# Kernel tuning notes

Hardware: AMD Instinct MI355X
Metric: run time of the kernel (lower is better)

## Reference

```python
import jax, jax.numpy as jnp
import numpy as np

N_G = 1024
H, W = 192, 256
FX, FY, CX, CY = 220.0, 220.0, 128.0, 96.0
NEAR, FAR = 0.01, 10.0
MARGIN = 0.1
ALPHA_THR = 1e-5
C0 = 0.28209479177387814
C1 = 0.4886025119029199
C2 = (1.0925484305920792, -1.0925484305920792, 0.31539156525252005, -1.0925484305920792, 0.5462742152960396)
C3 = (-0.5900435899266435, 2.890611442640554, -0.4570457994644658, 0.3731763325901154, -0.4570457994644658, 1.445305721320277, -0.5900435899266435)


def setup_inputs() -> dict:
    key = jax.random.key(0)
    k = jax.random.split(key, 6)
    xy = jax.random.uniform(k[0], (N_G, 2), minval=-1.5, maxval=1.5)
    z = jax.random.uniform(k[1], (N_G, 1), minval=0.5, maxval=6.0)
    positions = jnp.concatenate([xy, z], axis=1)
    rotations = jax.random.normal(k[2], (N_G, 4))
    scales = jnp.log(jax.random.uniform(k[3], (N_G, 3), minval=0.02, maxval=0.1))  # log-scale, as in module
    opacity = jax.random.uniform(k[4], (N_G, 1), minval=0.1, maxval=0.9)
    sh_coeffs = 0.3 * jax.random.normal(k[5], (N_G, 16, 3))
    T_WC = jnp.eye(4, dtype=jnp.float32)
    return {"positions": positions, "rotations": rotations, "scales": scales,
            "opacity": opacity, "sh_coeffs": sh_coeffs, "T_WC": T_WC}


def _quat_to_rot(q):
    q = q / (jnp.linalg.norm(q, axis=1, keepdims=True) + 1e-12)
    w, x, y, z = q[:, 0], q[:, 1], q[:, 2], q[:, 3]
    R = jnp.stack([
        1 - 2 * (y * y + z * z), 2 * (x * y - w * z), 2 * (x * z + w * y),
        2 * (x * y + w * z), 1 - 2 * (x * x + z * z), 2 * (y * z - w * x),
        2 * (x * z - w * y), 2 * (y * z + w * x), 1 - 2 * (x * x + y * y)], axis=1)
    return R.reshape(-1, 3, 3)


def _eval_sh(sh, d):
    # sh: [N,16,3] degree-3 SH, d: [N,3] unit view dirs (standard 3DGS real SH)
    x, y, z = d[:, 0:1], d[:, 1:2], d[:, 2:3]
    c = C0 * sh[:, 0] - C1 * y * sh[:, 1] + C1 * z * sh[:, 2] - C1 * x * sh[:, 3]
    xx, yy, zz = x * x, y * y, z * z
    xy, yz, xz = x * y, y * z, x * z
    c = c + C2[0] * xy * sh[:, 4] + C2[1] * yz * sh[:, 5] + C2[2] * (2 * zz - xx - yy) * sh[:, 6] \
          + C2[3] * xz * sh[:, 7] + C2[4] * (xx - yy) * sh[:, 8]
    c = c + C3[0] * y * (3 * xx - yy) * sh[:, 9] + C3[1] * xy * z * sh[:, 10] \
          + C3[2] * y * (4 * zz - xx - yy) * sh[:, 11] + C3[3] * z * (2 * zz - 3 * xx - 3 * yy) * sh[:, 12] \
          + C3[4] * x * (4 * zz - xx - yy) * sh[:, 13] + C3[5] * z * (xx - yy) * sh[:, 14] \
          + C3[6] * x * (xx - 3 * yy) * sh[:, 15]
    return jnp.clip(c + 0.5, 0.0, 1.0)


def _forward(positions, rotations, scales, opacity, sh_coeffs, T_WC):
    n = positions.shape[0]
    pts_h = jnp.concatenate([positions, jnp.ones((n, 1), positions.dtype)], axis=1)
    pc = (pts_h @ T_WC.T)[:, :3]  # world -> camera
    xs_c, ys_c, z = pc[:, 0], pc[:, 1], pc[:, 2]
    az = jnp.abs(z)
    x_fac = max(CX / FX, (W - CX) / FX)
    y_fac = max(CY / FY, (H - CY) / FY)
    valid = (az > NEAR) & (az < FAR) \
        & (jnp.abs(xs_c) < az * x_fac * (1 + MARGIN)) \
        & (jnp.abs(ys_c) < az * y_fac * (1 + MARGIN))
    zs = jnp.where(jnp.abs(z) < 1e-8, 1e-8, z)
    u = FX * xs_c / zs + CX
    v = FY * ys_c / zs + CY
    # 3D covariance Sigma = (R S)(R S)^T, then 2D via perspective Jacobian J Sigma J^T
    R = _quat_to_rot(rotations)
    S = jnp.exp(scales)  # scales stored in log space
    M = R * S[:, None, :]
    cov3d = jnp.einsum('nij,nkj->nik', M, M)
    zero = jnp.zeros_like(zs)
    J = jnp.stack([
        jnp.stack([FX / zs, zero, -FX * xs_c / (zs * zs)], axis=1),
        jnp.stack([zero, FY / zs, -FY * ys_c / (zs * zs)], axis=1)], axis=1)
    cov2d = jnp.einsum('nij,njk,nlk->nil', J, cov3d, J)
    a = cov2d[:, 0, 0] + 0.3  # low-pass dilation as in 3DGS
    b = cov2d[:, 0, 1]
    c = cov2d[:, 1, 1] + 0.3
    det = jnp.maximum(a * c - b * b, 1e-12)
    A, B, Cc = c / det, -b / det, a / det  # conic (inverse covariance)
    # frustum culling as mask: culled gaussians contribute zero opacity
    op = opacity[:, 0] * valid.astype(positions.dtype)
    dirs = pc / (jnp.linalg.norm(pc, axis=1, keepdims=True) + 1e-12)
    colors = _eval_sh(sh_coeffs, dirs)  # [N,3]
    # depth sort DESCENDING (as in module) -> back-to-front painter compositing
    order = jnp.argsort(-z)
    u, v, A, B, Cc, op, zd, colors = (t[order] for t in (u, v, A, B, Cc, op, z, colors))
    # dense per-pixel evaluation  [P, N]
    px = jnp.arange(W, dtype=positions.dtype) + 0.5
    py = jnp.arange(H, dtype=positions.dtype) + 0.5
    gx, gy = jnp.meshgrid(px, py)  # [H, W]
    gx, gy = gx.reshape(-1, 1), gy.reshape(-1, 1)
    dx = gx - u[None, :]
    dy = gy - v[None, :]
    power = -0.5 * (A[None, :] * dx * dx + Cc[None, :] * dy * dy) - B[None, :] * dx * dy
    alpha = jnp.minimum(0.99, op[None, :] * jnp.exp(jnp.minimum(power, 0.0)))
    alpha = jnp.where(alpha < ALPHA_THR, 0.0, alpha)
    # back-to-front: C = sum_i c_i a_i prod_{j>i} (1-a_j)  (exclusive suffix product)
    one_m = 1.0 - alpha
    cp = jnp.cumprod(one_m[:, ::-1], axis=1)
    T = jnp.concatenate([jnp.ones((alpha.shape[0], 1), alpha.dtype), cp[:, :-1]], axis=1)[:, ::-1]
    w = alpha * T
    rgb = (w @ colors).reshape(H, W, 3)
    depth = (w @ zd).reshape(H, W, 1)
    return rgb, depth


def reference(positions, rotations, scales, opacity, sh_coeffs, T_WC):
    return _forward(positions, rotations, scales, opacity, sh_coeffs, T_WC)
```

## Files before the change

### kernel.cpp

```cpp
#include <hip/hip_runtime.h>
#include <hip/hip_bf16.h>

#define NG 1024
#define IMW 256
#define IMH 192
#define NPIX (IMW*IMH)
#define FXc 220.0f
#define FYc 220.0f
#define CXc 128.0f
#define CYc 96.0f
#define NEARc 0.01f
#define FARc 10.0f
#define ALPHA_THRc 1e-5f

#define SH_C0 0.28209479177387814f
#define SH_C1 0.4886025119029199f
#define SH_C2_0 1.0925484305920792f
#define SH_C2_1 (-1.0925484305920792f)
#define SH_C2_2 0.31539156525252005f
#define SH_C2_3 (-1.0925484305920792f)
#define SH_C2_4 0.5462742152960396f
#define SH_C3_0 (-0.5900435899266435f)
#define SH_C3_1 2.890611442640554f
#define SH_C3_2 (-0.4570457994644658f)
#define SH_C3_3 0.3731763325901154f
#define SH_C3_4 (-0.4570457994644658f)
#define SH_C3_5 1.445305721320277f
#define SH_C3_6 (-0.5900435899266435f)


__global__ __launch_bounds__(64)
void gs_prep(const float* __restrict__ pos, const float* __restrict__ rot,
             const float* __restrict__ scl, const float* __restrict__ opac,
             const float* __restrict__ sh,  const float* __restrict__ Twc,
             float4* __restrict__ g0, float4* __restrict__ g1,
             float4* __restrict__ g2) {
    int i = blockIdx.x * 64 + threadIdx.x;
    if (i >= NG) return;

    float p0 = pos[i*3+0], p1 = pos[i*3+1], p2 = pos[i*3+2];
    float xc = Twc[0]*p0 + Twc[1]*p1 + Twc[2]*p2  + Twc[3];
    float yc = Twc[4]*p0 + Twc[5]*p1 + Twc[6]*p2  + Twc[7];
    float zc = Twc[8]*p0 + Twc[9]*p1 + Twc[10]*p2 + Twc[11];

    float az = fabsf(zc);
    const float xfac = fmaxf(CXc/FXc, (IMW - CXc)/FXc) * 1.1f;
    const float yfac = fmaxf(CYc/FYc, (IMH - CYc)/FYc) * 1.1f;
    bool valid = (az > NEARc) && (az < FARc) &&
                 (fabsf(xc) < az * xfac) && (fabsf(yc) < az * yfac);

    float zs = (az < 1e-8f) ? 1e-8f : zc;
    float iz = 1.0f / zs;
    float u = FXc * xc * iz + CXc;
    float v = FYc * yc * iz + CYc;

    float qw = rot[i*4+0], qx = rot[i*4+1], qy = rot[i*4+2], qz = rot[i*4+3];
    float qn = sqrtf(qw*qw + qx*qx + qy*qy + qz*qz) + 1e-12f;
    float inq = 1.0f / qn;
    qw *= inq; qx *= inq; qy *= inq; qz *= inq;
    float R00 = 1.0f - 2.0f*(qy*qy + qz*qz);
    float R01 = 2.0f*(qx*qy - qw*qz);
    float R02 = 2.0f*(qx*qz + qw*qy);
    float R10 = 2.0f*(qx*qy + qw*qz);
    float R11 = 1.0f - 2.0f*(qx*qx + qz*qz);
    float R12 = 2.0f*(qy*qz - qw*qx);
    float R20 = 2.0f*(qx*qz - qw*qy);
    float R21 = 2.0f*(qy*qz + qw*qx);
    float R22 = 1.0f - 2.0f*(qx*qx + qy*qy);

    float s0 = expf(scl[i*3+0]);
    float s1 = expf(scl[i*3+1]);
    float s2 = expf(scl[i*3+2]);
    float M00 = R00*s0, M01 = R01*s1, M02 = R02*s2;
    float M10 = R10*s0, M11 = R11*s1, M12 = R12*s2;
    float M20 = R20*s0, M21 = R21*s1, M22 = R22*s2;

    float S00 = M00*M00 + M01*M01 + M02*M02;
    float S01 = M00*M10 + M01*M11 + M02*M12;
    float S02 = M00*M20 + M01*M21 + M02*M22;
    float S11 = M10*M10 + M11*M11 + M12*M12;
    float S12 = M10*M20 + M11*M21 + M12*M22;
    float S22 = M20*M20 + M21*M21 + M22*M22;

    float j00 = FXc * iz,  j02 = -FXc * xc * iz * iz;
    float j11 = FYc * iz,  j12 = -FYc * yc * iz * iz;
    float c00 = j00*j00*S00 + 2.0f*j00*j02*S02 + j02*j02*S22 + 0.3f;
    float c01 = j00*j11*S01 + j00*j12*S02 + j02*j11*S12 + j02*j12*S22;
    float c11 = j11*j11*S11 + 2.0f*j11*j12*S12 + j12*j12*S22 + 0.3f;
    float det = fmaxf(c00*c11 - c01*c01, 1e-12f);
    float idet = 1.0f / det;
    float Ai = c11 * idet;
    float Bi = -c01 * idet;
    float Ci = c00 * idet;

    float op = valid ? opac[i] : 0.0f;

    float Q = fmaxf(2.0f * logf(fmaxf(op, 1e-20f) * 1e5f), 0.0f);
    float rx = valid ? (sqrtf(Q * c00) + 1e-3f) : -1e9f;
    float ry = valid ? (sqrtf(Q * c11) + 1e-3f) : -1e9f;

    float pn = sqrtf(xc*xc + yc*yc + zc*zc) + 1e-12f;
    float ipn = 1.0f / pn;
    float dx = xc*ipn, dy = yc*ipn, dz = zc*ipn;
    float xx = dx*dx, yy = dy*dy, zz = dz*dz;
    float xy = dx*dy, yz = dy*dz, xz = dx*dz;

    const float* s = sh + i*48;
    float col[3];
#pragma unroll
    for (int ch = 0; ch < 3; ++ch) {
        float c = SH_C0*s[0+ch] - SH_C1*dy*s[3+ch] + SH_C1*dz*s[6+ch] - SH_C1*dx*s[9+ch];
        c += SH_C2_0*xy*s[12+ch] + SH_C2_1*yz*s[15+ch] + SH_C2_2*(2.0f*zz-xx-yy)*s[18+ch]
           + SH_C2_3*xz*s[21+ch] + SH_C2_4*(xx-yy)*s[24+ch];
        c += SH_C3_0*dy*(3.0f*xx-yy)*s[27+ch] + SH_C3_1*xy*dz*s[30+ch]
           + SH_C3_2*dy*(4.0f*zz-xx-yy)*s[33+ch] + SH_C3_3*dz*(2.0f*zz-3.0f*xx-3.0f*yy)*s[36+ch]
           + SH_C3_4*dx*(4.0f*zz-xx-yy)*s[39+ch] + SH_C3_5*dz*(xx-yy)*s[42+ch]
           + SH_C3_6*dx*(xx-3.0f*yy)*s[45+ch];
        col[ch] = fminf(fmaxf(c + 0.5f, 0.0f), 1.0f);
    }

    g0[i] = make_float4(u, v, Ai, Bi);
    g1[i] = make_float4(Ci, op, col[0], col[1]);
    g2[i] = make_float4(col[2], zc, rx, ry);
}

__global__ __launch_bounds__(256)
void gs_tile(const float4* __restrict__ g0, const float4* __restrict__ g1,
             const float4* __restrict__ g2, float* __restrict__ out) {
    __shared__ float4 sv0[NG], sv1[NG], sv2[NG];
    __shared__ unsigned long long key[NG];
    __shared__ unsigned short ord[NG];
    __shared__ int scnt;

    int t = threadIdx.y * 16 + threadIdx.x;
    if (t == 0) scnt = 0;
    __syncthreads();

    float tx0 = (float)(blockIdx.x * 16) + 0.5f;
    float tx1 = tx0 + 15.0f;
    float ty0 = (float)(blockIdx.y * 16) + 0.5f;
    float ty1 = ty0 + 15.0f;

#pragma unroll
    for (int p = 0; p < 4; ++p) {
        int i = p * 256 + t;
        float4 a0 = g0[i];
        float4 a2 = g2[i];
        bool pass = (a0.x + a2.z >= tx0) && (a0.x - a2.z <= tx1) &&
                    (a0.y + a2.w >= ty0) && (a0.y - a2.w <= ty1);
        if (pass) {
            int pos = atomicAdd(&scnt, 1);
            sv0[pos] = a0;
            sv1[pos] = g1[i];
            sv2[pos] = a2;
            unsigned int zb = __float_as_uint(a2.y);
            zb = (zb & 0x80000000u) ? ~zb : (zb | 0x80000000u);
            key[pos] = ((unsigned long long)zb << 32) | (unsigned int)(NG - 1 - i);
        }
    }
    __syncthreads();
    int M = scnt;

    for (int s = t; s < M; s += 256) {
        unsigned long long ks = key[s];
        int rank = 0;
        for (int j = 0; j < M; ++j)
            rank += (key[j] < ks) ? 1 : 0;
        ord[rank] = (unsigned short)s;
    }
    __syncthreads();

    float px = tx0 + (float)threadIdx.x;
    float py = ty0 + (float)threadIdx.y;
    float T = 1.0f;
    float cr = 0.0f, cg = 0.0f, cb = 0.0f, cd = 0.0f;

#pragma unroll 2
    for (int j = 0; j < M; ++j) {
        int slot = ord[j];
        float4 a0 = sv0[slot];
        float4 a1 = sv1[slot];
        float4 a2 = sv2[slot];
        float dx = px - a0.x;
        float dy = py - a0.y;
        float pw = -0.5f * (a0.z * dx * dx + a1.x * dy * dy) - a0.w * dx * dy;
        pw = fminf(pw, 0.0f);
        float alpha = fminf(0.99f, a1.y * __expf(pw));
        float aeff = (alpha >= ALPHA_THRc) ? alpha : 0.0f;
        float w = aeff * T;
        cr += w * a1.z;
        cg += w * a1.w;
        cb += w * a2.x;
        cd += w * a2.y;
        T *= 1.0f - aeff;
        if (__all(T < 1e-4f)) break;
    }

    int x = blockIdx.x * 16 + threadIdx.x;
    int y = blockIdx.y * 16 + threadIdx.y;
    int idx = y * IMW + x;
    out[idx*3 + 0] = cr;
    out[idx*3 + 1] = cg;
    out[idx*3 + 2] = cb;
    out[NPIX*3 + idx] = cd;
}

extern "C" void kernel_launch(void* const* d_in, const int* in_sizes, int n_in,
                              void* d_out, int out_size, void* d_ws, size_t ws_size,
                              hipStream_t stream) {
    const float* pos  = (const float*)d_in[0];
    const float* rot  = (const float*)d_in[1];
    const float* scl  = (const float*)d_in[2];
    const float* opac = (const float*)d_in[3];
    const float* sh   = (const float*)d_in[4];
    const float* Twc  = (const float*)d_in[5];
    float* out = (float*)d_out;

    char* ws = (char*)d_ws;
    float4* g0 = (float4*)ws;
    float4* g1 = (float4*)(ws + 16384);
    float4* g2 = (float4*)(ws + 32768);

    gs_prep<<<dim3(NG/64), dim3(64), 0, stream>>>(pos, rot, scl, opac, sh, Twc,
                                                  g0, g1, g2);
    gs_tile<<<dim3(IMW/16, IMH/16), dim3(16, 16), 0, stream>>>(g0, g1, g2, out);
}
```

Baseline: 27.99 us.

## Use 8x8 single-wavefront tiles and pack colors/depth as fp16

Shrinks tiles from 16x16 pixels with 256 threads to 8x8 pixels with one 64-thread wavefront, giving 768 blocks instead of 192 so more of the GPU is busy. Smaller tiles also cull more Gaussians per tile and let early termination via __all apply per wavefront. Color and depth are packed as half2 into the second float4, removing the third shared array and one LDS load per Gaussian. The fp16 depth also feeds the sort key, which loses precision, can change back-to-front ordering, and lowers the accuracy of the depth output.

```diff
diff --git a/kernel.cpp b/kernel.cpp
--- a/kernel.cpp
+++ b/kernel.cpp
@@ -1,5 +1,6 @@
 #include <hip/hip_runtime.h>
 #include <hip/hip_bf16.h>
+#include <hip/hip_fp16.h>
 
 #define NG 1024
 #define IMW 256
@@ -34,7 +35,7 @@
              const float* __restrict__ scl, const float* __restrict__ opac,
              const float* __restrict__ sh,  const float* __restrict__ Twc,
              float4* __restrict__ g0, float4* __restrict__ g1,
-             float4* __restrict__ g2) {
+             float2* __restrict__ g2) {
     int i = blockIdx.x * 64 + threadIdx.x;
     if (i >= NG) return;
 
@@ -119,41 +120,45 @@
         col[ch] = fminf(fmaxf(c + 0.5f, 0.0f), 1.0f);
     }
 
+    __half2 rg = __floats2half2_rn(col[0], col[1]);
+    __half2 bz = __floats2half2_rn(col[2], zc);
+
     g0[i] = make_float4(u, v, Ai, Bi);
-    g1[i] = make_float4(Ci, op, col[0], col[1]);
-    g2[i] = make_float4(col[2], zc, rx, ry);
+    g1[i] = make_float4(Ci, op, __uint_as_float(*(unsigned int*)&rg),
+                                __uint_as_float(*(unsigned int*)&bz));
+    g2[i] = make_float2(rx, ry);
 }
 
-__global__ __launch_bounds__(256)
+__global__ __launch_bounds__(64)
 void gs_tile(const float4* __restrict__ g0, const float4* __restrict__ g1,
-             const float4* __restrict__ g2, float* __restrict__ out) {
-    __shared__ float4 sv0[NG], sv1[NG], sv2[NG];
+             const float2* __restrict__ g2, float* __restrict__ out) {
+    __shared__ float4 sv0[NG], sv1[NG];
     __shared__ unsigned long long key[NG];
     __shared__ unsigned short ord[NG];
     __shared__ int scnt;
 
-    int t = threadIdx.y * 16 + threadIdx.x;
+    int t = threadIdx.x;
     if (t == 0) scnt = 0;
     __syncthreads();
 
-    float tx0 = (float)(blockIdx.x * 16) + 0.5f;
-    float tx1 = tx0 + 15.0f;
-    float ty0 = (float)(blockIdx.y * 16) + 0.5f;
-    float ty1 = ty0 + 15.0f;
-
-#pragma unroll
-    for (int p = 0; p < 4; ++p) {
-        int i = p * 256 + t;
+    float tx0 = (float)(blockIdx.x * 8) + 0.5f;
+    float tx1 = tx0 + 7.0f;
+    float ty0 = (float)(blockIdx.y * 8) + 0.5f;
+    float ty1 = ty0 + 7.0f;
+
+#pragma unroll 4
+    for (int p = 0; p < 16; ++p) {
+        int i = p * 64 + t;
         float4 a0 = g0[i];
-        float4 a2 = g2[i];
-        bool pass = (a0.x + a2.z >= tx0) && (a0.x - a2.z <= tx1) &&
-                    (a0.y + a2.w >= ty0) && (a0.y - a2.w <= ty1);
+        float2 a2 = g2[i];
+        bool pass = (a0.x + a2.x >= tx0) && (a0.x - a2.x <= tx1) &&
+                    (a0.y + a2.y >= ty0) && (a0.y - a2.y <= ty1);
         if (pass) {
             int pos = atomicAdd(&scnt, 1);
             sv0[pos] = a0;
-            sv1[pos] = g1[i];
-            sv2[pos] = a2;
-            unsigned int zb = __float_as_uint(a2.y);
+            float4 a1 = g1[i];
+            sv1[pos] = a1;
+            unsigned int zb = __float_as_uint(__high2float(*(__half2*)&a1.w));
             zb = (zb & 0x80000000u) ? ~zb : (zb | 0x80000000u);
             key[pos] = ((unsigned long long)zb << 32) | (unsigned int)(NG - 1 - i);
         }
@@ -161,7 +166,7 @@
     __syncthreads();
     int M = scnt;
 
-    for (int s = t; s < M; s += 256) {
+    for (int s = t; s < M; s += 64) {
         unsigned long long ks = key[s];
         int rank = 0;
         for (int j = 0; j < M; ++j)
@@ -170,8 +175,8 @@
     }
     __syncthreads();
 
-    float px = tx0 + (float)threadIdx.x;
-    float py = ty0 + (float)threadIdx.y;
+    float px = tx0 + (float)(t & 7);
+    float py = ty0 + (float)(t >> 3);
     float T = 1.0f;
     float cr = 0.0f, cg = 0.0f, cb = 0.0f, cd = 0.0f;
 
@@ -180,7 +185,6 @@
         int slot = ord[j];
         float4 a0 = sv0[slot];
         float4 a1 = sv1[slot];
-        float4 a2 = sv2[slot];
         float dx = px - a0.x;
         float dy = py - a0.y;
         float pw = -0.5f * (a0.z * dx * dx + a1.x * dy * dy) - a0.w * dx * dy;
@@ -188,16 +192,18 @@
         float alpha = fminf(0.99f, a1.y * __expf(pw));
         float aeff = (alpha >= ALPHA_THRc) ? alpha : 0.0f;
         float w = aeff * T;
-        cr += w * a1.z;
-        cg += w * a1.w;
-        cb += w * a2.x;
-        cd += w * a2.y;
+        float2 rg = __half22float2(*(__half2*)&a1.z);
+        float2 bz = __half22float2(*(__half2*)&a1.w);
+        cr += w * rg.x;
+        cg += w * rg.y;
+        cb += w * bz.x;
+        cd += w * bz.y;
         T *= 1.0f - aeff;
         if (__all(T < 1e-4f)) break;
     }
 
-    int x = blockIdx.x * 16 + threadIdx.x;
-    int y = blockIdx.y * 16 + threadIdx.y;
+    int x = blockIdx.x * 8 + (t & 7);
+    int y = blockIdx.y * 8 + (t >> 3);
     int idx = y * IMW + x;
     out[idx*3 + 0] = cr;
     out[idx*3 + 1] = cg;
@@ -219,9 +225,9 @@
     char* ws = (char*)d_ws;
     float4* g0 = (float4*)ws;
     float4* g1 = (float4*)(ws + 16384);
-    float4* g2 = (float4*)(ws + 32768);
+    float2* g2 = (float2*)(ws + 32768);
 
     gs_prep<<<dim3(NG/64), dim3(64), 0, stream>>>(pos, rot, scl, opac, sh, Twc,
                                                   g0, g1, g2);
-    gs_tile<<<dim3(IMW/16, IMH/16), dim3(16, 16), 0, stream>>>(g0, g1, g2, out);
+    gs_tile<<<dim3(IMW/8, IMH/8), dim3(64), 0, stream>>>(g0, g1, g2, out);
 }
```

Result: slower. 29.66 us (+5.9%).

## Fuse Gaussian preprocessing into tile rasterizer with fp16-packed colors

Applied to the files above, without the earlier changes.

Removes the separate preprocessing kernel: each 16x16 tile block recomputes projection and covariance for all 1024 Gaussians and keeps only those overlapping the tile. SH color is evaluated only for the survivors during the sort pass. Colors and depth are packed as half2 into one float4, which cuts shared memory from three float4 arrays to two. This saves a kernel launch and the global round trip, but every one of the 192 blocks repeats the per-Gaussian math, and depth and color lose precision in fp16.

```diff
diff --git a/kernel.cpp b/kernel.cpp
--- a/kernel.cpp
+++ b/kernel.cpp
@@ -1,5 +1,6 @@
 #include <hip/hip_runtime.h>
 #include <hip/hip_bf16.h>
+#include <hip/hip_fp16.h>
 
 #define NG 1024
 #define IMW 256
@@ -28,111 +29,18 @@
 #define SH_C3_5 1.445305721320277f
 #define SH_C3_6 (-0.5900435899266435f)
 
-
-__global__ __launch_bounds__(64)
-void gs_prep(const float* __restrict__ pos, const float* __restrict__ rot,
-             const float* __restrict__ scl, const float* __restrict__ opac,
-             const float* __restrict__ sh,  const float* __restrict__ Twc,
-             float4* __restrict__ g0, float4* __restrict__ g1,
-             float4* __restrict__ g2) {
-    int i = blockIdx.x * 64 + threadIdx.x;
-    if (i >= NG) return;
-
-    float p0 = pos[i*3+0], p1 = pos[i*3+1], p2 = pos[i*3+2];
-    float xc = Twc[0]*p0 + Twc[1]*p1 + Twc[2]*p2  + Twc[3];
-    float yc = Twc[4]*p0 + Twc[5]*p1 + Twc[6]*p2  + Twc[7];
-    float zc = Twc[8]*p0 + Twc[9]*p1 + Twc[10]*p2 + Twc[11];
-
-    float az = fabsf(zc);
-    const float xfac = fmaxf(CXc/FXc, (IMW - CXc)/FXc) * 1.1f;
-    const float yfac = fmaxf(CYc/FYc, (IMH - CYc)/FYc) * 1.1f;
-    bool valid = (az > NEARc) && (az < FARc) &&
-                 (fabsf(xc) < az * xfac) && (fabsf(yc) < az * yfac);
-
-    float zs = (az < 1e-8f) ? 1e-8f : zc;
-    float iz = 1.0f / zs;
-    float u = FXc * xc * iz + CXc;
-    float v = FYc * yc * iz + CYc;
-
-    float qw = rot[i*4+0], qx = rot[i*4+1], qy = rot[i*4+2], qz = rot[i*4+3];
-    float qn = sqrtf(qw*qw + qx*qx + qy*qy + qz*qz) + 1e-12f;
-    float inq = 1.0f / qn;
-    qw *= inq; qx *= inq; qy *= inq; qz *= inq;
-    float R00 = 1.0f - 2.0f*(qy*qy + qz*qz);
-    float R01 = 2.0f*(qx*qy - qw*qz);
-    float R02 = 2.0f*(qx*qz + qw*qy);
-    float R10 = 2.0f*(qx*qy + qw*qz);
-    float R11 = 1.0f - 2.0f*(qx*qx + qz*qz);
-    float R12 = 2.0f*(qy*qz - qw*qx);
-    float R20 = 2.0f*(qx*qz - qw*qy);
-    float R21 = 2.0f*(qy*qz + qw*qx);
-    float R22 = 1.0f - 2.0f*(qx*qx + qy*qy);
-
-    float s0 = expf(scl[i*3+0]);
-    float s1 = expf(scl[i*3+1]);
-    float s2 = expf(scl[i*3+2]);
-    float M00 = R00*s0, M01 = R01*s1, M02 = R02*s2;
-    float M10 = R10*s0, M11 = R11*s1, M12 = R12*s2;
-    float M20 = R20*s0, M21 = R21*s1, M22 = R22*s2;
-
-    float S00 = M00*M00 + M01*M01 + M02*M02;
-    float S01 = M00*M10 + M01*M11 + M02*M12;
-    float S02 = M00*M20 + M01*M21 + M02*M22;
-    float S11 = M10*M10 + M11*M11 + M12*M12;
-    float S12 = M10*M20 + M11*M21 + M12*M22;
-    float S22 = M20*M20 + M21*M21 + M22*M22;
-
-    float j00 = FXc * iz,  j02 = -FXc * xc * iz * iz;
-    float j11 = FYc * iz,  j12 = -FYc * yc * iz * iz;
-    float c00 = j00*j00*S00 + 2.0f*j00*j02*S02 + j02*j02*S22 + 0.3f;
-    float c01 = j00*j11*S01 + j00*j12*S02 + j02*j11*S12 + j02*j12*S22;
-    float c11 = j11*j11*S11 + 2.0f*j11*j12*S12 + j12*j12*S22 + 0.3f;
-    float det = fmaxf(c00*c11 - c01*c01, 1e-12f);
-    float idet = 1.0f / det;
-    float Ai = c11 * idet;
-    float Bi = -c01 * idet;
-    float Ci = c00 * idet;
-
-    float op = valid ? opac[i] : 0.0f;
-
-    float Q = fmaxf(2.0f * logf(fmaxf(op, 1e-20f) * 1e5f), 0.0f);
-    float rx = valid ? (sqrtf(Q * c00) + 1e-3f) : -1e9f;
-    float ry = valid ? (sqrtf(Q * c11) + 1e-3f) : -1e9f;
-
-    float pn = sqrtf(xc*xc + yc*yc + zc*zc) + 1e-12f;
-    float ipn = 1.0f / pn;
-    float dx = xc*ipn, dy = yc*ipn, dz = zc*ipn;
-    float xx = dx*dx, yy = dy*dy, zz = dz*dz;
-    float xy = dx*dy, yz = dy*dz, xz = dx*dz;
-
-    const float* s = sh + i*48;
-    float col[3];
-#pragma unroll
-    for (int ch = 0; ch < 3; ++ch) {
-        float c = SH_C0*s[0+ch] - SH_C1*dy*s[3+ch] + SH_C1*dz*s[6+ch] - SH_C1*dx*s[9+ch];
-        c += SH_C2_0*xy*s[12+ch] + SH_C2_1*yz*s[15+ch] + SH_C2_2*(2.0f*zz-xx-yy)*s[18+ch]
-           + SH_C2_3*xz*s[21+ch] + SH_C2_4*(xx-yy)*s[24+ch];
-        c += SH_C3_0*dy*(3.0f*xx-yy)*s[27+ch] + SH_C3_1*xy*dz*s[30+ch]
-           + SH_C3_2*dy*(4.0f*zz-xx-yy)*s[33+ch] + SH_C3_3*dz*(2.0f*zz-3.0f*xx-3.0f*yy)*s[36+ch]
-           + SH_C3_4*dx*(4.0f*zz-xx-yy)*s[39+ch] + SH_C3_5*dz*(xx-yy)*s[42+ch]
-           + SH_C3_6*dx*(xx-3.0f*yy)*s[45+ch];
-        col[ch] = fminf(fmaxf(c + 0.5f, 0.0f), 1.0f);
-    }
-
-    g0[i] = make_float4(u, v, Ai, Bi);
-    g1[i] = make_float4(Ci, op, col[0], col[1]);
-    g2[i] = make_float4(col[2], zc, rx, ry);
-}
-
 __global__ __launch_bounds__(256)
-void gs_tile(const float4* __restrict__ g0, const float4* __restrict__ g1,
-             const float4* __restrict__ g2, float* __restrict__ out) {
-    __shared__ float4 sv0[NG], sv1[NG], sv2[NG];
+void gs_fused(const float* __restrict__ pos, const float* __restrict__ rot,
+              const float* __restrict__ scl, const float* __restrict__ opac,
+              const float* __restrict__ sh,  const float* __restrict__ Twc,
+              float* __restrict__ out) {
+    __shared__ float4 sv0[NG];
+    __shared__ float4 sv1[NG];
     __shared__ unsigned long long key[NG];
     __shared__ unsigned short ord[NG];
     __shared__ int scnt;
 
-    int t = threadIdx.y * 16 + threadIdx.x;
+    int t = threadIdx.x;
     if (t == 0) scnt = 0;
     __syncthreads();
 
@@ -141,22 +49,81 @@
     float ty0 = (float)(blockIdx.y * 16) + 0.5f;
     float ty1 = ty0 + 15.0f;
 
-#pragma unroll
+    float T0 = Twc[0],  T1 = Twc[1],  T2 = Twc[2],  T3 = Twc[3];
+    float T4 = Twc[4],  T5 = Twc[5],  T6 = Twc[6],  T7 = Twc[7];
+    float T8 = Twc[8],  T9 = Twc[9],  T10 = Twc[10], T11 = Twc[11];
+
+    const float xfac = fmaxf(CXc/FXc, (IMW - CXc)/FXc) * 1.1f;
+    const float yfac = fmaxf(CYc/FYc, (IMH - CYc)/FYc) * 1.1f;
+
     for (int p = 0; p < 4; ++p) {
         int i = p * 256 + t;
-        float4 a0 = g0[i];
-        float4 a2 = g2[i];
-        bool pass = (a0.x + a2.z >= tx0) && (a0.x - a2.z <= tx1) &&
-                    (a0.y + a2.w >= ty0) && (a0.y - a2.w <= ty1);
-        if (pass) {
-            int pos = atomicAdd(&scnt, 1);
-            sv0[pos] = a0;
-            sv1[pos] = g1[i];
-            sv2[pos] = a2;
-            unsigned int zb = __float_as_uint(a2.y);
-            zb = (zb & 0x80000000u) ? ~zb : (zb | 0x80000000u);
-            key[pos] = ((unsigned long long)zb << 32) | (unsigned int)(NG - 1 - i);
-        }
+        float p0 = pos[i*3+0], p1 = pos[i*3+1], p2 = pos[i*3+2];
+        float xc = T0*p0 + T1*p1 + T2*p2  + T3;
+        float yc = T4*p0 + T5*p1 + T6*p2  + T7;
+        float zc = T8*p0 + T9*p1 + T10*p2 + T11;
+        float az = fabsf(zc);
+        bool valid = (az > NEARc) && (az < FARc) &&
+                     (fabsf(xc) < az * xfac) && (fabsf(yc) < az * yfac);
+        float op = opac[i];
+        if (!(valid && op > 0.0f)) continue;
+
+        float zs = (az < 1e-8f) ? 1e-8f : zc;
+        float iz = 1.0f / zs;
+        float u = FXc * xc * iz + CXc;
+        float v = FYc * yc * iz + CYc;
+
+        float qw = rot[i*4+0], qx = rot[i*4+1], qy = rot[i*4+2], qz = rot[i*4+3];
+        float qn = sqrtf(qw*qw + qx*qx + qy*qy + qz*qz) + 1e-12f;
+        float inq = 1.0f / qn;
+        qw *= inq; qx *= inq; qy *= inq; qz *= inq;
+        float R00 = 1.0f - 2.0f*(qy*qy + qz*qz);
+        float R01 = 2.0f*(qx*qy - qw*qz);
+        float R02 = 2.0f*(qx*qz + qw*qy);
+        float R10 = 2.0f*(qx*qy + qw*qz);
+        float R11 = 1.0f - 2.0f*(qx*qx + qz*qz);
+        float R12 = 2.0f*(qy*qz - qw*qx);
+        float R20 = 2.0f*(qx*qz - qw*qy);
+        float R21 = 2.0f*(qy*qz + qw*qx);
+        float R22 = 1.0f - 2.0f*(qx*qx + qy*qy);
+
+        float s0 = expf(scl[i*3+0]);
+        float s1 = expf(scl[i*3+1]);
+        float s2 = expf(scl[i*3+2]);
+        float M00 = R00*s0, M01 = R01*s1, M02 = R02*s2;
+        float M10 = R10*s0, M11 = R11*s1, M12 = R12*s2;
+        float M20 = R20*s0, M21 = R21*s1, M22 = R22*s2;
+
+        float S00 = M00*M00 + M01*M01 + M02*M02;
+        float S01 = M00*M10 + M01*M11 + M02*M12;
+        float S02 = M00*M20 + M01*M21 + M02*M22;
+        float S11 = M10*M10 + M11*M11 + M12*M12;
+        float S12 = M10*M20 + M11*M21 + M12*M22;
+        float S22 = M20*M20 + M21*M21 + M22*M22;
+
+        float j00 = FXc * iz,  j02 = -FXc * xc * iz * iz;
+        float j11 = FYc * iz,  j12 = -FYc * yc * iz * iz;
+        float c00 = j00*j00*S00 + 2.0f*j00*j02*S02 + j02*j02*S22 + 0.3f;
+        float c01 = j00*j11*S01 + j00*j12*S02 + j02*j11*S12 + j02*j12*S22;
+        float c11 = j11*j11*S11 + 2.0f*j11*j12*S12 + j12*j12*S22 + 0.3f;
+
+        float Q = fmaxf(2.0f * logf(fmaxf(op, 1e-20f) * 1e5f), 0.0f);
+        float rx = sqrtf(Q * c00) + 1e-3f;
+        float ry = sqrtf(Q * c11) + 1e-3f;
+
+        bool pass = (u + rx >= tx0) && (u - rx <= tx1) &&
+                    (v + ry >= ty0) && (v - ry <= ty1);
+        if (!pass) continue;
+
+        float det = fmaxf(c00*c11 - c01*c01, 1e-12f);
+        float idet = 1.0f / det;
+
+        int slot = atomicAdd(&scnt, 1);
+        sv0[slot] = make_float4(u, v, c11*idet, -c01*idet);
+        sv1[slot] = make_float4(c00*idet, op, xc, yc);
+        unsigned int zb = __float_as_uint(zc);
+        zb = (zb & 0x80000000u) ? ~zb : (zb | 0x80000000u);
+        key[slot] = ((unsigned long long)zb << 32) | (unsigned int)(NG - 1 - i);
     }
     __syncthreads();
     int M = scnt;
@@ -166,38 +133,69 @@
         int rank = 0;
         for (int j = 0; j < M; ++j)
             rank += (key[j] < ks) ? 1 : 0;
+
+        unsigned int zb = (unsigned int)(ks >> 32);
+        unsigned int zorig = (zb & 0x80000000u) ? (zb & 0x7fffffffu) : ~zb;
+        float zc = __uint_as_float(zorig);
+        int i = NG - 1 - (int)(ks & 0xFFFFFFFFu);
+        float4 a1 = sv1[s];
+        float xc = a1.z, yc = a1.w;
+
+        float pn = sqrtf(xc*xc + yc*yc + zc*zc) + 1e-12f;
+        float ipn = 1.0f / pn;
+        float dx = xc*ipn, dy = yc*ipn, dz = zc*ipn;
+        float xx = dx*dx, yy = dy*dy, zz = dz*dz;
+        float xy = dx*dy, yz = dy*dz, xz = dx*dz;
+
+        const float* sp = sh + i*48;
+        float col[3];
+#pragma unroll
+        for (int ch = 0; ch < 3; ++ch) {
+            float c = SH_C0*sp[0+ch] - SH_C1*dy*sp[3+ch] + SH_C1*dz*sp[6+ch] - SH_C1*dx*sp[9+ch];
+            c += SH_C2_0*xy*sp[12+ch] + SH_C2_1*yz*sp[15+ch] + SH_C2_2*(2.0f*zz-xx-yy)*sp[18+ch]
+               + SH_C2_3*xz*sp[21+ch] + SH_C2_4*(xx-yy)*sp[24+ch];
+            c += SH_C3_0*dy*(3.0f*xx-yy)*sp[27+ch] + SH_C3_1*xy*dz*sp[30+ch]
+               + SH_C3_2*dy*(4.0f*zz-xx-yy)*sp[33+ch] + SH_C3_3*dz*(2.0f*zz-3.0f*xx-3.0f*yy)*sp[36+ch]
+               + SH_C3_4*dx*(4.0f*zz-xx-yy)*sp[39+ch] + SH_C3_5*dz*(xx-yy)*sp[42+ch]
+               + SH_C3_6*dx*(xx-3.0f*yy)*sp[45+ch];
+            col[ch] = fminf(fmaxf(c + 0.5f, 0.0f), 1.0f);
+        }
+        __half2 rg = __floats2half2_rn(col[0], col[1]);
+        __half2 bz = __floats2half2_rn(col[2], zc);
+        sv1[s] = make_float4(a1.x, a1.y, __uint_as_float(*(unsigned int*)&rg),
+                                          __uint_as_float(*(unsigned int*)&bz));
         ord[rank] = (unsigned short)s;
     }
     __syncthreads();
 
-    float px = tx0 + (float)threadIdx.x;
-    float py = ty0 + (float)threadIdx.y;
+    float px = tx0 + (float)(t & 15);
+    float py = ty0 + (float)(t >> 4);
     float T = 1.0f;
     float cr = 0.0f, cg = 0.0f, cb = 0.0f, cd = 0.0f;
 
-#pragma unroll 2
     for (int j = 0; j < M; ++j) {
         int slot = ord[j];
-        float4 a0 = sv0[slot];
-        float4 a1 = sv1[slot];
-        float4 a2 = sv2[slot];
-        float dx = px - a0.x;
-        float dy = py - a0.y;
-        float pw = -0.5f * (a0.z * dx * dx + a1.x * dy * dy) - a0.w * dx * dy;
+        float4 b0 = sv0[slot];
+        float4 b1 = sv1[slot];
+        float dx = px - b0.x;
+        float dy = py - b0.y;
+        float pw = -0.5f * (b0.z * dx * dx + b1.x * dy * dy) - b0.w * dx * dy;
         pw = fminf(pw, 0.0f);
-        float alpha = fminf(0.99f, a1.y * __expf(pw));
+        float alpha = fminf(0.99f, b1.y * __expf(pw));
         float aeff = (alpha >= ALPHA_THRc) ? alpha : 0.0f;
         float w = aeff * T;
-        cr += w * a1.z;
-        cg += w * a1.w;
-        cb += w * a2.x;
-        cd += w * a2.y;
+        float2 rg = __half22float2(*(__half2*)&b1.z);
+        float2 bz = __half22float2(*(__half2*)&b1.w);
+        cr += w * rg.x;
+        cg += w * rg.y;
+        cb += w * bz.x;
+        cd += w * bz.y;
         T *= 1.0f - aeff;
         if (__all(T < 1e-4f)) break;
     }
 
-    int x = blockIdx.x * 16 + threadIdx.x;
-    int y = blockIdx.y * 16 + threadIdx.y;
+    int x = blockIdx.x * 16 + (t & 15);
+    int y = blockIdx.y * 16 + (t >> 4);
     int idx = y * IMW + x;
     out[idx*3 + 0] = cr;
     out[idx*3 + 1] = cg;
@@ -216,12 +214,6 @@
     const float* Twc  = (const float*)d_in[5];
     float* out = (float*)d_out;
 
-    char* ws = (char*)d_ws;
-    float4* g0 = (float4*)ws;
-    float4* g1 = (float4*)(ws + 16384);
-    float4* g2 = (float4*)(ws + 32768);
-
-    gs_prep<<<dim3(NG/64), dim3(64), 0, stream>>>(pos, rot, scl, opac, sh, Twc,
-                                                  g0, g1, g2);
-    gs_tile<<<dim3(IMW/16, IMH/16), dim3(16, 16), 0, stream>>>(g0, g1, g2, out);
+    gs_fused<<<dim3(IMW/16, IMH/16), dim3(256), 0, stream>>>(
+        pos, rot, scl, opac, sh, Twc, out);
 }
```

New measurement: 26.94 us. 1.04x faster.
